# Optimization experiments

Hardware: AMD Instinct MI355X
Metric: run time of the kernel (lower is better)

The kernel has to match this reference:

```python
import jax, jax.numpy as jnp
import numpy as np

OFR = 2.0      # offset_range_factor
WSIZE = 8      # window_size
SPLIT = 1      # split_size


def _grid_sample(img, grid):
    # torch.nn.functional.grid_sample: bilinear, align_corners=True, padding_mode='zeros'
    # img: (B,C,H,W); grid: (B,Gh,Gw,2) with (x,y) in [-1,1]
    B, C, H, W = img.shape
    gx = (grid[..., 0] + 1.0) * 0.5 * (W - 1)
    gy = (grid[..., 1] + 1.0) * 0.5 * (H - 1)
    x0 = jnp.floor(gx)
    y0 = jnp.floor(gy)
    wx1 = gx - x0
    wy1 = gy - y0
    imgf = img.reshape(B, C, H * W)

    def corner(yc, xc, wgt):
        valid = (xc >= 0) & (xc <= W - 1) & (yc >= 0) & (yc <= H - 1)
        idx = (jnp.clip(yc, 0, H - 1) * W + jnp.clip(xc, 0, W - 1)).astype(jnp.int32)
        g = jnp.take_along_axis(imgf, idx.reshape(B, 1, -1), axis=2)  # (B,C,N)
        return g * (wgt * valid).reshape(B, 1, -1)

    out = (corner(y0, x0, (1 - wy1) * (1 - wx1)) + corner(y0, x0 + 1, (1 - wy1) * wx1)
           + corner(y0 + 1, x0, wy1 * (1 - wx1)) + corner(y0 + 1, x0 + 1, wy1 * wx1))
    return out.reshape(B, C, *grid.shape[1:-1])


def _win_attn(xqv, dh, dw):
    # 'b (qv c) (h dh) (w dw) -> qv (b h w) (dh dw) c' ; dot attention ; inverse rearrange
    B, cc, H, W = xqv.shape
    c = cc // 2
    t = xqv.reshape(B, 2, c, H // dh, dh, W // dw, dw)
    t = t.transpose(1, 0, 3, 5, 4, 6, 2).reshape(2, -1, dh * dw, c)
    q, v = t[0], t[1]
    atn = jax.nn.softmax(q @ jnp.swapaxes(q, -1, -2), axis=-1)
    o = atn @ v  # (nw, dh*dw, c)
    o = o.reshape(B, H // dh, W // dw, dh, dw, c).transpose(0, 5, 1, 3, 2, 4).reshape(B, c, H, W)
    return o


def setup_inputs() -> dict:
    key = jax.random.key(0)
    ks = jax.random.split(key, 16)
    C, B, H, W = 48, 2, 64, 64
    rn = lambda k, s, sc=0.05: (jax.random.normal(k, s) * sc).astype(jnp.float32)
    return {
        'x': jax.random.normal(ks[0], (B, C, H, W), jnp.float32),
        'Wq': rn(ks[1], (C, C)), 'bq': rn(ks[2], (C,)),
        'off_dw_w': rn(ks[3], (C, 1, 3, 3)), 'off_dw_b': rn(ks[4], (C,)),
        'off_ln_g': jnp.ones((C,), jnp.float32), 'off_ln_b': jnp.zeros((C,), jnp.float32),
        'off_pw_w': rn(ks[5], (2, C)),
        'Wk': rn(ks[6], (C, C)), 'bk': rn(ks[7], (C,)),
        'Wv': rn(ks[8], (C, C)), 'bv': rn(ks[9], (C,)),
        'inp_w': rn(ks[10], (2 * C, C)), 'inp_b': rn(ks[11], (2 * C,)),
        'bn_g': jnp.ones((2 * C,), jnp.float32), 'bn_b': jnp.zeros((2 * C,), jnp.float32),
        'bn_mean': jnp.zeros((2 * C,), jnp.float32), 'bn_var': jnp.ones((2 * C,), jnp.float32),
        'pout_w': rn(ks[12], (C, C)), 'pout_b': rn(ks[13], (C,)),
        'rpe': rn(ks[14], (1, 191, 191), 0.01),  # 96*2-1
    }


def reference(x, Wq, bq, off_dw_w, off_dw_b, off_ln_g, off_ln_b, off_pw_w, Wk, bk, Wv, bv,
              inp_w, inp_b, bn_g, bn_b, bn_mean, bn_var, pout_w, pout_b, rpe):
    B, C, h, w = x.shape
    scale = C ** (-0.5)
    c1 = lambda t, W_, b_=None: jnp.einsum('oc,bchw->bohw', W_, t) + (0.0 if b_ is None else b_[None, :, None, None])
    q = c1(x, Wq, bq)
    # conv_offset: depthwise 3x3 -> LayerNorm over channels -> GELU -> 1x1 to 2 ch (no bias)
    t = jax.lax.conv_general_dilated(q, off_dw_w, (1, 1), ((1, 1), (1, 1)),
                                     dimension_numbers=('NCHW', 'OIHW', 'NCHW'),
                                     feature_group_count=C) + off_dw_b[None, :, None, None]
    mu = t.mean(1, keepdims=True)
    var = ((t - mu) ** 2).mean(1, keepdims=True)
    t = (t - mu) * jax.lax.rsqrt(var + 1e-5) * off_ln_g[None, :, None, None] + off_ln_b[None, :, None, None]
    t = jax.nn.gelu(t, approximate=False)
    offset = c1(t, off_pw_w)  # (B,2,h,w), channel 0 = y, 1 = x
    n = h * w
    orange = jnp.array([1.0 / (h - 1), 1.0 / (w - 1)], jnp.float32).reshape(1, 2, 1, 1)
    offset = jnp.tanh(offset) * orange * OFR
    offset = offset.transpose(0, 2, 3, 1)  # (B,h,w,2) (y,x)
    ry = jnp.linspace(0.5, h - 0.5, h) / (h - 1) * 2.0 - 1.0
    rx = jnp.linspace(0.5, w - 0.5, w) / (w - 1) * 2.0 - 1.0
    ref = jnp.stack(jnp.meshgrid(ry, rx, indexing='ij'), -1)[None]
    pos = offset + ref  # (B,h,w,2) (y,x)
    x_sampled = _grid_sample(x, pos[..., ::-1]).reshape(B, C, n)
    # project_inp: 1x1 conv -> BatchNorm2d (eval mode)
    x2 = c1(x, inp_w, inp_b)
    x2 = (x2 - bn_mean[None, :, None, None]) * jax.lax.rsqrt(bn_var + 1e-5)[None, :, None, None] \
         * bn_g[None, :, None, None] + bn_b[None, :, None, None]
    s = 2 * C // 3
    xs0, xs1, xs2 = x2[:, :s], x2[:, s:2 * s], x2[:, 2 * s:]
    # deformable global attention
    qf = q.reshape(B, C, n)
    k = jnp.einsum('oc,bcn->bon', Wk, x_sampled) + bk[None, :, None]
    v = jnp.einsum('oc,bcn->bon', Wv, x_sampled) + bv[None, :, None]
    attn = jnp.einsum('bcm,bcn->bmn', qf, k) * scale
    gy = jnp.arange(h, dtype=jnp.float32) / (h - 1) * 2.0 - 1.0
    gx = jnp.arange(w, dtype=jnp.float32) / (w - 1) * 2.0 - 1.0
    qg = jnp.stack(jnp.meshgrid(gy, gx, indexing='ij'), -1).reshape(n, 2)
    disp = (qg[None, :, None, :] - pos.reshape(B, n, 2)[:, None, :, :]) * 0.5  # (B,m,n,2) (y,x)
    rpe_img = jnp.broadcast_to(rpe[None], (B,) + rpe.shape)  # (B,1,191,191)
    attn_bias = _grid_sample(rpe_img, disp[..., ::-1]).reshape(B, n, n)
    attn = jax.nn.softmax(attn + attn_bias, axis=2)
    out_dat = jnp.einsum('bmn,bcn->bcm', attn, v).reshape(B, C, h, w)
    # windowed / column / row local attention (shifts=0)
    out = jnp.concatenate([_win_attn(xs0, WSIZE, WSIZE),
                           _win_attn(xs1, h, SPLIT),
                           _win_attn(xs2, SPLIT, w)], axis=1)
    out = c1(out, pout_w, pout_b)
    return out * 0.5 + out_dat * 0.5
```

## Files before the change

kernel.cpp:

```cpp
#include <hip/hip_runtime.h>
#include <hip/hip_bf16.h>
#include <math.h>

#define Bsz 2
#define Cch 48
#define Hh 64
#define Ww 64
#define Nn 4096

typedef __bf16 bf16;
typedef __attribute__((ext_vector_type(8))) __bf16 bf16x8;
typedef __attribute__((ext_vector_type(4))) float f32x4;

#define LOG2E 1.44269504088896340736f

__device__ __forceinline__ float fast_exp2(float x){
#if __has_builtin(__builtin_amdgcn_exp2f)
  return __builtin_amdgcn_exp2f(x);
#else
  return exp2f(x);
#endif
}

__global__ void k_conv1x1(const float* __restrict__ in, const float* __restrict__ Wt,
                          const float* __restrict__ bias, float* __restrict__ qnc,
                          bf16* __restrict__ qbf, float* __restrict__ xt,
                          const float* __restrict__ rpe,
                          unsigned* __restrict__ rpe2){
  if (blockIdx.x >= Bsz * Cch * 16){
    int y = blockIdx.x - Bsz * Cch * 16;
    for (int j = threadIdx.x; j < 312; j += 256){
      int xcol = j - 48;
      float lo = 0.f, hi = 0.f;
      if (xcol >= 0 && xcol < 191){
        if (y >= 1 && y < 192) lo = rpe[(y - 1) * 191 + xcol] * LOG2E;
        if (y < 191)           hi = rpe[y * 191 + xcol] * LOG2E;
      }
      unsigned ulo = __builtin_bit_cast(unsigned short, (bf16)lo);
      unsigned uhi = __builtin_bit_cast(unsigned short, (bf16)hi);
      rpe2[y * 312 + j] = (uhi << 16) | ulo;
    }
    return;
  }
  int chunk = blockIdx.x & 15;
  int o = (blockIdx.x >> 4) % Cch;
  int b = blockIdx.x / (16 * Cch);
  int p = chunk * 256 + threadIdx.x;
  float acc = bias[o];
  const float* ip = in + (b * Cch) * Nn + p;
  const float* wp = Wt + o * Cch;
  #pragma unroll
  for (int c = 0; c < Cch; c++) acc += wp[c] * ip[c * Nn];
  qnc[((size_t)(b * Nn + p)) * 48 + o] = acc;
  xt [((size_t)(b * Nn + p)) * 48 + o] = ip[o * Nn];
  size_t qb = ((size_t)(b * Nn + p)) * 64;
  qbf[qb + o] = (bf16)acc;
  if (o < 16) qbf[qb + 48 + o] = (bf16)0.f;
}

__global__ __launch_bounds__(512) void k_pos_kv(const float* __restrict__ qnc,
                           const float* __restrict__ dww, const float* __restrict__ dwb,
                           const float* __restrict__ lng, const float* __restrict__ lnb,
                           const float* __restrict__ pww,
                           const float* __restrict__ xt,
                           const float* __restrict__ Wk, const float* __restrict__ bk,
                           const float* __restrict__ Wv, const float* __restrict__ bv,
                           bf16* __restrict__ kk2, bf16* __restrict__ vt2,
                           float2* __restrict__ axay){
  __shared__ float wkt[48][49];
  __shared__ float wvt[48][49];
  __shared__ float rowb[8][48];
  int tid = threadIdx.x;
  for (int f = tid; f < 2304; f += 512){
    int o = f / 48, c = f - o * 48;
    wkt[c][o] = Wk[f];
    wvt[c][o] = Wv[f];
  }
  __syncthreads();
  int wv = tid >> 6, lane = tid & 63;
  int idx = blockIdx.x * 8 + wv;
  int b = idx >> 12;
  int n = idx & (Nn - 1);
  int yq = n >> 6, xq = n & 63;
  int c = lane;
  float t = 0.f;
  if (c < 48){
    t = dwb[c];
    #pragma unroll
    for (int ky = -1; ky <= 1; ky++){
      int yy = yq + ky;
      if (yy < 0 || yy >= Hh) continue;
      #pragma unroll
      for (int kx = -1; kx <= 1; kx++){
        int xx = xq + kx;
        if (xx < 0 || xx >= Ww) continue;
        t = fmaf(qnc[((size_t)(b * Nn + yy * Ww + xx)) * 48 + c],
                 dww[c * 9 + (ky + 1) * 3 + (kx + 1)], t);
      }
    }
  }
  float s = t;
  #pragma unroll
  for (int m = 1; m < 64; m <<= 1) s += __shfl_xor(s, m);
  float mean = s * (1.f / 48.f);
  float d = (c < 48) ? (t - mean) : 0.f;
  float v = d * d;
  #pragma unroll
  for (int m = 1; m < 64; m <<= 1) v += __shfl_xor(v, m);
  float rstd = rsqrtf(v * (1.f / 48.f) + 1e-5f);
  float p0 = 0.f, p1 = 0.f;
  if (c < 48){
    float u = (t - mean) * rstd * lng[c] + lnb[c];
    u = 0.5f * u * (1.f + erff(u * 0.70710678118654752f));
    p0 = pww[c] * u;
    p1 = pww[48 + c] * u;
  }
  #pragma unroll
  for (int m = 1; m < 64; m <<= 1){ p0 += __shfl_xor(p0, m); p1 += __shfl_xor(p1, m); }
  float py = tanhf(p0) * (2.f / 63.f) + ((0.5f + (float)yq) * (2.f / 63.f) - 1.f);
  float px = tanhf(p1) * (2.f / 63.f) + ((0.5f + (float)xq) * (2.f / 63.f) - 1.f);
  if (lane == 0) axay[idx] = make_float2(95.f - 47.5f * py, 95.f - 47.5f * px);
  float gx = (px + 1.f) * 0.5f * 63.f;
  float gy = (py + 1.f) * 0.5f * 63.f;
  float x0f = floorf(gx), y0f = floorf(gy);
  float wx = gx - x0f, wy = gy - y0f;
  int x0 = (int)x0f, y0 = (int)y0f, x1 = x0 + 1, y1 = y0 + 1;
  float w00 = (1.f - wy) * (1.f - wx), w01 = (1.f - wy) * wx;
  float w10 = wy * (1.f - wx),         w11 = wy * wx;
  bool vx0 = (x0 >= 0) && (x0 < Ww), vx1 = (x1 >= 0) && (x1 < Ww);
  bool vy0 = (y0 >= 0) && (y0 < Hh), vy1 = (y1 >= 0) && (y1 < Hh);
  if (!(vx0 && vy0)) w00 = 0.f;
  if (!(vx1 && vy0)) w01 = 0.f;
  if (!(vx0 && vy1)) w10 = 0.f;
  if (!(vx1 && vy1)) w11 = 0.f;
  int cx0 = min(max(x0, 0), Ww - 1), cx1 = min(max(x1, 0), Ww - 1);
  int cy0 = min(max(y0, 0), Hh - 1), cy1 = min(max(y1, 0), Hh - 1);
  int i00 = cy0 * Ww + cx0, i01 = cy0 * Ww + cx1;
  int i10 = cy1 * Ww + cx0, i11 = cy1 * Ww + cx1;
  if (c < 48){
    const float* t00 = xt + (size_t)(b * Nn + i00) * 48;
    const float* t01 = xt + (size_t)(b * Nn + i01) * 48;
    const float* t10 = xt + (size_t)(b * Nn + i10) * 48;
    const float* t11 = xt + (size_t)(b * Nn + i11) * 48;
    rowb[wv][c] = w00 * t00[c] + w01 * t01[c] + w10 * t10[c] + w11 * t11[c];
  }
  int o = lane;
  if (o < 48){
    float ka = bk[o], va = bv[o];
    #pragma unroll
    for (int cc = 0; cc < 48; cc++){
      float r = rowb[wv][cc];
      ka = fmaf(wkt[cc][o], r, ka);
      va = fmaf(wvt[cc][o], r, va);
    }
    kk2[((((size_t)b * 256 + (n >> 4)) * 8 + (o >> 3)) * 16 + (n & 15)) * 8 + (o & 7)]
        = (bf16)ka;
    vt2[((size_t)b * 128 + (n >> 5)) * 1536 + (o >> 4) * 512 + (o & 15) * 32
        + ((n >> 3) & 3) * 8 + (n & 7)] = (bf16)va;
  }
  if (o < 16)
    kk2[((((size_t)b * 256 + (n >> 4)) * 8 + 6 + (o >> 3)) * 16 + (n & 15)) * 8 + (o & 7)]
        = (bf16)0.f;
}

__global__ __launch_bounds__(256, 5) void k_attn_win(const bf16* __restrict__ q_bf,
                                              const bf16* __restrict__ kk2,
                                              const bf16* __restrict__ vt2,
                                              const float2* __restrict__ axay,
                                              const unsigned* __restrict__ rpe2,
                                              float* __restrict__ o_part,
                                              float* __restrict__ s_part,
                                              const float* __restrict__ x,
                                              const float* __restrict__ iw,
                                              const float* __restrict__ ib,
                                              const float* __restrict__ bng,
                                              const float* __restrict__ bnb,
                                              const float* __restrict__ bnm,
                                              const float* __restrict__ bnv,
                                              float* __restrict__ wout){
  __shared__ __align__(16) char smem[25600];
  const int tid = threadIdx.x;
  const int wid = tid >> 6, lane = tid & 63;
  const int q16 = lane >> 4, l16 = lane & 15;

  if (blockIdx.x < 1024){
    float (*g)[26] = (float(*)[26])smem;
    float* axs  = (float*)(smem + 13312);
    float* wy0s = (float*)(smem + 14336);
    float* wy1s = (float*)(smem + 14848);
    int*   pbs  = (int*)  (smem + 15360);
    bf16 (*ps)[136] = (bf16(*)[136])(smem + 16384);

    const int b  = blockIdx.x >> 9;
    const int kp = (blockIdx.x >> 8) & 1;
    const int m0 = (blockIdx.x & 255) * 16;
    const int wn0 = wid * 32;

    const bf16* qb = q_bf + ((size_t)(b * Nn + m0 + l16)) * 64;
    bf16x8 qf0 = *(const bf16x8*)(qb + q16 * 8);
    bf16x8 qf1 = *(const bf16x8*)(qb + 32 + q16 * 8);

    const float qgy = (float)(m0 >> 6) * (2.f / 63.f) - 1.f;
    const float byq = 47.5f * qgy;
    const float scale2 = 0.14433756729740643f * LOG2E;
    const float bx0 = 47.5f * ((float)(m0 & 63) * (2.f / 63.f) - 1.f);
    float bxr[4];
    #pragma unroll
    for (int r = 0; r < 4; r++){
      int mcol = (m0 & 63) + q16 * 4 + r;
      bxr[r] = 47.5f * ((float)mcol * (2.f / 63.f) - 1.f);
    }

    f32x4 oacc[3];
    #pragma unroll
    for (int ct = 0; ct < 3; ct++) oacc[ct] = (f32x4){0.f, 0.f, 0.f, 0.f};
    float s_runw[4] = {0.f, 0.f, 0.f, 0.f};

    for (int chk = 0; chk < 16; chk++){
      const int n0 = kp * 2048 + chk * 128;
      if (lane < 32){
        int n = wn0 + lane;
        float2 aa = axay[(size_t)b * Nn + n0 + n];
        float gyr = aa.x + byq;
        float y0f = floorf(gyr);
        float wy = gyr - y0f;
        int y0 = (int)y0f, y1 = y0 + 1;
        wy0s[n] = ((unsigned)y0 < 191u) ? (1.f - wy) : 0.f;
        wy1s[n] = ((unsigned)y1 < 191u) ? wy : 0.f;
        int xlo = (int)floorf(aa.y + bx0);
        int t = min(max(y0 + 1, 0), 192);
        pbs[n] = t * 312 + xlo + 48;
        axs[n] = aa.y - (float)xlo;
      }
      {
        int s = lane >> 5, jj = lane & 31;
        if (jj < 26){
          #pragma unroll
          for (int it = 0; it < 16; it++){
            int n = wn0 + it * 2 + s;
            unsigned u = rpe2[pbs[n] + jj];
            float lo = __builtin_bit_cast(float, u << 16);
            float hi = __builtin_bit_cast(float, u & 0xffff0000u);
            g[n][jj] = wy0s[n] * lo + wy1s[n] * hi;
          }
        }
      }
      f32x4 s0 = (f32x4){0.f, 0.f, 0.f, 0.f};
      f32x4 s1 = (f32x4){0.f, 0.f, 0.f, 0.f};
      {
        const bf16* kbase = kk2 + (((size_t)b * 256 + ((n0 + wn0) >> 4)) << 10);
        bf16x8 b00 = *(const bf16x8*)(kbase + lane * 8);
        bf16x8 b01 = *(const bf16x8*)(kbase + 512 + lane * 8);
        bf16x8 b10 = *(const bf16x8*)(kbase + 1024 + lane * 8);
        bf16x8 b11 = *(const bf16x8*)(kbase + 1536 + lane * 8);
        s0 = __builtin_amdgcn_mfma_f32_16x16x32_bf16(qf0, b00, s0, 0, 0, 0);
        s0 = __builtin_amdgcn_mfma_f32_16x16x32_bf16(qf1, b01, s0, 0, 0, 0);
        s1 = __builtin_amdgcn_mfma_f32_16x16x32_bf16(qf0, b10, s1, 0, 0, 0);
        s1 = __builtin_amdgcn_mfma_f32_16x16x32_bf16(qf1, b11, s1, 0, 0, 0);
      }
      #pragma unroll
      for (int nt = 0; nt < 2; nt++){
        int nl = wn0 + nt * 16 + l16;
        float axf = axs[nl];
        f32x4 sv = nt ? s1 : s0;
        #pragma unroll
        for (int r = 0; r < 4; r++){
          float gxr = axf + bxr[r];
          int j0 = (int)gxr;
          float wx = gxr - (float)j0;
          float g0 = g[nl][j0], g1 = g[nl][j0 + 1];
          float bias = fmaf(wx, g1 - g0, g0);
          float e = fast_exp2(fmaf(sv[r], scale2, bias));
          s_runw[r] += e;
          ps[q16 * 4 + r][nl] = (bf16)e;
        }
      }
      {
        bf16x8 pa = *(const bf16x8*)&ps[l16][wn0 + q16 * 8];
        const bf16* vbase = vt2 + ((size_t)b * 128 + ((n0 + wn0) >> 5)) * 1536
                          + l16 * 32 + q16 * 8;
        #pragma unroll
        for (int ct = 0; ct < 3; ct++){
          bf16x8 vb = *(const bf16x8*)(vbase + ct * 512);
          oacc[ct] = __builtin_amdgcn_mfma_f32_16x16x32_bf16(pa, vb, oacc[ct], 0, 0, 0);
        }
      }
    }
    #pragma unroll
    for (int r = 0; r < 4; r++){
      #pragma unroll
      for (int msk = 1; msk < 16; msk <<= 1)
        s_runw[r] += __shfl_xor(s_runw[r], msk);
    }
    __syncthreads();
    float* ored = (float*)g;
    float* sred = axs;
    #pragma unroll
    for (int ct = 0; ct < 3; ct++)
      #pragma unroll
      for (int r = 0; r < 4; r++)
        ored[(wid * 16 + q16 * 4 + r) * 48 + ct * 16 + l16] = oacc[ct][r];
    if (l16 == 0){
      #pragma unroll
      for (int r = 0; r < 4; r++) sred[wid * 16 + q16 * 4 + r] = s_runw[r];
    }
    __syncthreads();
    size_t obase = ((size_t)(b * 2 + kp) * Cch) * Nn;
    #pragma unroll
    for (int e = 0; e < 3; e++){
      int idx = tid + e * 256;
      int c = idx >> 4, mm = idx & 15;
      float v = ored[mm * 48 + c] + ored[(16 + mm) * 48 + c]
              + ored[(32 + mm) * 48 + c] + ored[(48 + mm) * 48 + c];
      o_part[obase + (size_t)c * Nn + m0 + mm] = v;
    }
    if (tid < 16)
      s_part[(size_t)(b * 2 + kp) * Nn + m0 + tid] =
          sred[tid] + sred[16 + tid] + sred[32 + tid] + sred[48 + tid];
  } else {
    bf16 (*xs)[72]  = (bf16(*)[72])smem;
    bf16 (*wtt)[72] = (bf16(*)[72])(smem + 9216);
    bf16 (*qs)[72]  = (bf16(*)[72])(smem + 13824);
    bf16 (*vst)[72] = (bf16(*)[72])(smem + 23040);
    float* bnsc = (float*)(smem + 25344);
    float* bnsh = (float*)(smem + 25472);
    bf16 (*psw)[72] = xs;

    int wb = blockIdx.x - 1024;
    int s = wb >> 7;
    int r7 = wb & 127;
    int b = r7 >> 6, wi = r7 & 63;
    for (int f = tid; f < 64 * 48; f += 256){
      int t = f & 63, c = f >> 6;
      int p = (s == 0) ? (((wi >> 3) * 8 + (t >> 3)) * 64 + (wi & 7) * 8 + (t & 7))
            : (s == 1) ? (t * 64 + wi) : (wi * 64 + t);
      xs[t][c] = (bf16)x[((size_t)(b * 48 + c)) * Nn + p];
    }
    for (int f = tid; f < 64 * 16; f += 256){
      int t = f >> 4, j = f & 15;
      xs[t][48 + j] = (bf16)0.f;
      qs[t][16 + j] = (bf16)0.f;
    }
    for (int f = tid; f < 32 * 64; f += 256){
      int o = f >> 6, c = f & 63;
      wtt[o][c] = (c < 48) ? (bf16)iw[(s * 32 + o) * 48 + c] : (bf16)0.f;
    }
    if (tid < 32){
      int ch = s * 32 + tid;
      float sc = bng[ch] * rsqrtf(bnv[ch] + 1e-5f);
      bnsc[tid] = sc;
      bnsh[tid] = (ib[ch] - bnm[ch]) * sc + bnb[ch];
    }
    __syncthreads();
    {
      bf16x8 a0 = *(const bf16x8*)&xs[wid * 16 + l16][q16 * 8];
      bf16x8 a1 = *(const bf16x8*)&xs[wid * 16 + l16][32 + q16 * 8];
      #pragma unroll
      for (int nt = 0; nt < 2; nt++){
        bf16x8 b0 = *(const bf16x8*)&wtt[nt * 16 + l16][q16 * 8];
        bf16x8 b1 = *(const bf16x8*)&wtt[nt * 16 + l16][32 + q16 * 8];
        f32x4 acc = (f32x4){0.f, 0.f, 0.f, 0.f};
        acc = __builtin_amdgcn_mfma_f32_16x16x32_bf16(a0, b0, acc, 0, 0, 0);
        acc = __builtin_amdgcn_mfma_f32_16x16x32_bf16(a1, b1, acc, 0, 0, 0);
        float scv = bnsc[nt * 16 + l16], shv = bnsh[nt * 16 + l16];
        #pragma unroll
        for (int r = 0; r < 4; r++){
          float v = fmaf(acc[r], scv, shv);
          int tok = wid * 16 + q16 * 4 + r;
          if (nt == 0) qs[tok][l16] = (bf16)v;
          else         vst[l16][tok] = (bf16)v;
        }
      }
    }
    __syncthreads();
    f32x4 sreg[4];
    {
      bf16x8 aq = *(const bf16x8*)&qs[wid * 16 + l16][q16 * 8];
      #pragma unroll
      for (int nt = 0; nt < 4; nt++){
        bf16x8 bq = *(const bf16x8*)&qs[nt * 16 + l16][q16 * 8];
        f32x4 acc = (f32x4){0.f, 0.f, 0.f, 0.f};
        sreg[nt] = __builtin_amdgcn_mfma_f32_16x16x32_bf16(aq, bq, acc, 0, 0, 0);
      }
    }
    float rinv[4];
    #pragma unroll
    for (int r = 0; r < 4; r++){
      float mx = fmaxf(fmaxf(sreg[0][r], sreg[1][r]), fmaxf(sreg[2][r], sreg[3][r]));
      #pragma unroll
      for (int msk = 1; msk < 16; msk <<= 1) mx = fmaxf(mx, __shfl_xor(mx, msk));
      float sum = 0.f;
      #pragma unroll
      for (int nt = 0; nt < 4; nt++){
        float e = __expf(sreg[nt][r] - mx);
        sum += e;
        psw[wid * 16 + q16 * 4 + r][nt * 16 + l16] = (bf16)e;
      }
      #pragma unroll
      for (int msk = 1; msk < 16; msk <<= 1) sum += __shfl_xor(sum, msk);
      rinv[r] = 1.f / sum;
    }
    f32x4 oac = (f32x4){0.f, 0.f, 0.f, 0.f};
    {
      bf16x8 pa0 = *(const bf16x8*)&psw[wid * 16 + l16][q16 * 8];
      bf16x8 pa1 = *(const bf16x8*)&psw[wid * 16 + l16][32 + q16 * 8];
      bf16x8 vb0 = *(const bf16x8*)&vst[l16][q16 * 8];
      bf16x8 vb1 = *(const bf16x8*)&vst[l16][32 + q16 * 8];
      oac = __builtin_amdgcn_mfma_f32_16x16x32_bf16(pa0, vb0, oac, 0, 0, 0);
      oac = __builtin_amdgcn_mfma_f32_16x16x32_bf16(pa1, vb1, oac, 0, 0, 0);
    }
    #pragma unroll
    for (int r = 0; r < 4; r++){
      int tok = wid * 16 + q16 * 4 + r;
      int p = (s == 0) ? (((wi >> 3) * 8 + (tok >> 3)) * 64 + (wi & 7) * 8 + (tok & 7))
            : (s == 1) ? (tok * 64 + wi) : (wi * 64 + tok);
      wout[((size_t)(b * 48 + s * 16 + l16)) * Nn + p] = oac[r] * rinv[r];
    }
  }
}

__global__ void k_final(const float* __restrict__ win, const float* __restrict__ pw,
                        const float* __restrict__ pb, const float* __restrict__ o_part,
                        const float* __restrict__ s_part, float* __restrict__ out){
  int chunk = blockIdx.x & 15;
  int o = (blockIdx.x >> 4) % Cch;
  int b = blockIdx.x / (16 * Cch);
  int p = chunk * 256 + threadIdx.x;
  float acc = pb[o];
  const float* ip = win + (b * Cch) * Nn + p;
  const float* wp = pw + o * Cch;
  #pragma unroll
  for (int c = 0; c < Cch; c++) acc += wp[c] * ip[c * Nn];
  float sden = s_part[(size_t)(b * 2) * Nn + p] + s_part[(size_t)(b * 2 + 1) * Nn + p];
  float odv = (o_part[((size_t)(b * 2) * Cch + o) * Nn + p]
             + o_part[((size_t)(b * 2 + 1) * Cch + o) * Nn + p]) / sden;
  out[(b * Cch + o) * Nn + p] = 0.5f * acc + 0.5f * odv;
}

extern "C" void kernel_launch(void* const* d_in, const int* in_sizes, int n_in,
                              void* d_out, int out_size, void* d_ws, size_t ws_size,
                              hipStream_t stream){
  const float* x   = (const float*)d_in[0];
  const float* Wq  = (const float*)d_in[1];
  const float* bq  = (const float*)d_in[2];
  const float* dww = (const float*)d_in[3];
  const float* dwb = (const float*)d_in[4];
  const float* lng = (const float*)d_in[5];
  const float* lnb = (const float*)d_in[6];
  const float* pww = (const float*)d_in[7];
  const float* Wk  = (const float*)d_in[8];
  const float* bk  = (const float*)d_in[9];
  const float* Wv  = (const float*)d_in[10];
  const float* bv  = (const float*)d_in[11];
  const float* iw  = (const float*)d_in[12];
  const float* ib  = (const float*)d_in[13];
  const float* bng = (const float*)d_in[14];
  const float* bnb = (const float*)d_in[15];
  const float* bnm = (const float*)d_in[16];
  const float* bnv = (const float*)d_in[17];
  const float* pw  = (const float*)d_in[18];
  const float* pb  = (const float*)d_in[19];
  const float* rpe = (const float*)d_in[20];

  float*    ws     = (float*)d_ws;
  float*    qnc    = ws;
  float*    o_part = ws;
  float2*   axay   = (float2*)(ws + 802816);
  float*    wout   = ws + 819200;
  bf16*     q_bf   = (bf16*)(ws + 1212416);
  bf16*     kk2    = (bf16*)(ws + 1474560);
  bf16*     vt2    = (bf16*)(ws + 1736704);
  float*    s_part = ws + 1933312;
  unsigned* rpe2   = (unsigned*)(ws + 1949696);
  float*    x_t    = ws + 2009912;
  float*    out    = (float*)d_out;

  k_conv1x1 <<<Bsz * Cch * 16 + 193, 256, 0, stream>>>(x, Wq, bq, qnc, q_bf, x_t,
                                                       rpe, rpe2);
  k_pos_kv  <<<(Bsz * Nn) / 8, 512, 0, stream>>>(qnc, dww, dwb, lng, lnb, pww,
                                                 x_t, Wk, bk, Wv, bv,
                                                 kk2, vt2, axay);
  k_attn_win<<<Bsz * 512 + 384, 256, 0, stream>>>(q_bf, kk2, vt2, axay, rpe2,
                                                  o_part, s_part,
                                                  x, iw, ib, bng, bnb, bnm, bnv, wout);
  k_final   <<<Bsz * Cch * 16, 256, 0, stream>>>(wout, pw, pb, o_part,
                                                 s_part, out);
}
```

Before: 167.7 us.

## Restructure 1x1 conv so each thread computes all output channels per pixel

The Q projection kernel now assigns one pixel per thread and computes all 48 output channels from 48 input values held in registers, with weights and bias staged in shared memory. Before, each thread computed a single output channel and re-read all inputs, which meant scattered strided stores. The transposed x, fp32 q and bf16 q rows are now written as contiguous float4 and bf16x8 vector stores. The trade-off is heavy register use and only 128 compute blocks of 64 threads, so the GPU will be poorly occupied.

```diff
diff --git a/kernel.cpp b/kernel.cpp
--- a/kernel.cpp
+++ b/kernel.cpp
@@ -22,14 +22,15 @@
 #endif
 }
 
-__global__ void k_conv1x1(const float* __restrict__ in, const float* __restrict__ Wt,
+__global__ __launch_bounds__(64) void k_conv1x1(const float* __restrict__ in,
+                          const float* __restrict__ Wt,
                           const float* __restrict__ bias, float* __restrict__ qnc,
                           bf16* __restrict__ qbf, float* __restrict__ xt,
                           const float* __restrict__ rpe,
                           unsigned* __restrict__ rpe2){
-  if (blockIdx.x >= Bsz * Cch * 16){
-    int y = blockIdx.x - Bsz * Cch * 16;
-    for (int j = threadIdx.x; j < 312; j += 256){
+  if (blockIdx.x >= Bsz * 64){
+    int y = blockIdx.x - Bsz * 64;
+    for (int j = threadIdx.x; j < 312; j += 64){
       int xcol = j - 48;
       float lo = 0.f, hi = 0.f;
       if (xcol >= 0 && xcol < 191){
@@ -42,20 +43,44 @@
     }
     return;
   }
-  int chunk = blockIdx.x & 15;
-  int o = (blockIdx.x >> 4) % Cch;
-  int b = blockIdx.x / (16 * Cch);
-  int p = chunk * 256 + threadIdx.x;
-  float acc = bias[o];
-  const float* ip = in + (b * Cch) * Nn + p;
-  const float* wp = Wt + o * Cch;
-  #pragma unroll
-  for (int c = 0; c < Cch; c++) acc += wp[c] * ip[c * Nn];
-  qnc[((size_t)(b * Nn + p)) * 48 + o] = acc;
-  xt [((size_t)(b * Nn + p)) * 48 + o] = ip[o * Nn];
+  __shared__ float wS[48][48];
+  __shared__ float bS[48];
+  int tid = threadIdx.x;
+  for (int f = tid; f < 2304; f += 64) wS[f / 48][f % 48] = Wt[f];
+  if (tid < 48) bS[tid] = bias[tid];
+  __syncthreads();
+  int b = blockIdx.x >> 6;
+  int p = (blockIdx.x & 63) * 64 + tid;
+  float xv[48];
+  const float* xp = in + (size_t)(b * Cch) * Nn + p;
+  #pragma unroll
+  for (int c = 0; c < 48; c++) xv[c] = xp[c * Nn];
+  size_t base = ((size_t)(b * Nn + p)) * 48;
+  #pragma unroll
+  for (int og = 0; og < 12; og++)
+    *(float4*)(xt + base + og * 4) =
+        make_float4(xv[og * 4], xv[og * 4 + 1], xv[og * 4 + 2], xv[og * 4 + 3]);
+  bf16 qv[64];
+  #pragma unroll
+  for (int og = 0; og < 12; og++){
+    float a[4];
+    #pragma unroll
+    for (int r = 0; r < 4; r++){
+      int o = og * 4 + r;
+      float acc = bS[o];
+      #pragma unroll
+      for (int c = 0; c < 48; c++) acc += wS[o][c] * xv[c];
+      a[r] = acc;
+      qv[o] = (bf16)acc;
+    }
+    *(float4*)(qnc + base + og * 4) = make_float4(a[0], a[1], a[2], a[3]);
+  }
+  #pragma unroll
+  for (int o = 48; o < 64; o++) qv[o] = (bf16)0.f;
   size_t qb = ((size_t)(b * Nn + p)) * 64;
-  qbf[qb + o] = (bf16)acc;
-  if (o < 16) qbf[qb + 48 + o] = (bf16)0.f;
+  #pragma unroll
+  for (int v8 = 0; v8 < 8; v8++)
+    *(bf16x8*)(qbf + qb + v8 * 8) = *(bf16x8*)&qv[v8 * 8];
 }
 
 __global__ __launch_bounds__(512) void k_pos_kv(const float* __restrict__ qnc,
@@ -475,8 +500,8 @@
   float*    x_t    = ws + 2009912;
   float*    out    = (float*)d_out;
 
-  k_conv1x1 <<<Bsz * Cch * 16 + 193, 256, 0, stream>>>(x, Wq, bq, qnc, q_bf, x_t,
-                                                       rpe, rpe2);
+  k_conv1x1 <<<Bsz * 64 + 193, 64, 0, stream>>>(x, Wq, bq, qnc, q_bf, x_t,
+                                                rpe, rpe2);
   k_pos_kv  <<<(Bsz * Nn) / 8, 512, 0, stream>>>(qnc, dww, dwb, lng, lnb, pww,
                                                  x_t, Wk, bk, Wv, bv,
                                                  kk2, vt2, axay);
```

New measurement: 182.4 us. 8.8% more time.
